# Performance work log

Measured on AMD Instinct MI355X. Metric: run time of the kernel, lower is better.

## Reference

```python
import jax, jax.numpy as jnp
import numpy as np

NUM_PERTS = 20000
D = 256          # embedding_dim
B, C = 64, 512   # batch_size, num_cells
EPS = 1e-5


def setup_inputs() -> dict:
    key = jax.random.key(0)
    ks = jax.random.split(key, 20)
    inp = {
        'perturbation_ids': jax.random.randint(ks[0], (B, C), 0, NUM_PERTS),
        'table': jax.random.normal(ks[1], (NUM_PERTS, D), dtype=jnp.float32),
    }
    s = 1.0 / np.sqrt(D)
    for i in range(4):
        inp[f'W{i+1}'] = jax.random.uniform(ks[2 + 2 * i], (D, D), minval=-s, maxval=s, dtype=jnp.float32)
        inp[f'b{i+1}'] = jax.random.uniform(ks[3 + 2 * i], (D,), minval=-s, maxval=s, dtype=jnp.float32)
    for i in range(3):
        inp[f'g{i+1}'] = jnp.ones((D,), jnp.float32)
        inp[f'be{i+1}'] = jnp.zeros((D,), jnp.float32)
    return inp


def _bn(x, gamma, beta):
    # BatchNorm1d forward with batch statistics (training-mode math, biased var)
    mu = jnp.mean(x, axis=0)
    var = jnp.mean(jnp.square(x - mu), axis=0)
    return (x - mu) * jax.lax.rsqrt(var + EPS) * gamma + beta


def reference(perturbation_ids, table,
              W1, b1, W2, b2, W3, b3, W4, b4,
              g1, be1, g2, be2, g3, be3):
    # Vectorized replacement of the Python double-loop dict gather
    emb = table[perturbation_ids]                 # (B, C, D)
    x = emb.reshape(-1, D)                        # (B*C, D)
    x = _bn(jax.nn.gelu(x @ W1 + b1, approximate=False), g1, be1)
    x = _bn(jax.nn.gelu(x @ W2 + b2, approximate=False), g2, be2)
    x = _bn(jax.nn.gelu(x @ W3 + b3, approximate=False), g3, be3)
    x = jax.nn.gelu(x @ W4 + b4, approximate=False)
    return x.reshape(B, C, D)
```

## Files before the change

### kernel.cpp

```cpp
#include <hip/hip_runtime.h>
#include <math.h>


typedef __attribute__((ext_vector_type(8))) short short8;
typedef __attribute__((ext_vector_type(4))) float floatx4;

#define DDIM 256
#define NBLK 512

struct Params {
    const int* ids;
    const float* table;
    const float* b[4];
    const float* g[3];
    const float* be[3];
    const unsigned short* Wt;
    float* stats;
    unsigned int* barrier;
    float* out;
};

__device__ __forceinline__ unsigned short f2bf(float f) {
    union { float f; unsigned int u; } v; v.f = f;
    unsigned int r = v.u + 0x7fffu + ((v.u >> 16) & 1u);
    return (unsigned short)(r >> 16);
}
__device__ __forceinline__ float bf2f(unsigned short u) {
    union { unsigned int i; float f; } v; v.i = ((unsigned int)u) << 16;
    return v.f;
}
__device__ __forceinline__ float gelu_fast(float x) {
    float z = 0.7978845608f * (x + 0.044715f * x * x * x);
    float e = __expf(2.0f * z);
    float th = 1.0f - 2.0f * __builtin_amdgcn_rcpf(1.0f + e);
    return 0.5f * x * (1.0f + th);
}

__global__ __launch_bounds__(256) void prep_kernel(
    const float* __restrict__ W0, const float* __restrict__ W1,
    const float* __restrict__ W2, const float* __restrict__ W3,
    unsigned short* __restrict__ Wt, float* __restrict__ stats,
    unsigned int* __restrict__ barrier)
{
    __shared__ unsigned short T[64][68];
    const int t = threadIdx.x, b = blockIdx.x;
    const int j  = b >> 4;
    const int kr = ((b >> 2) & 3) * 64;
    const int nc = (b & 3) * 64;
    const float* W = (j == 0) ? W0 : (j == 1) ? W1 : (j == 2) ? W2 : W3;

    {
        const int k = t >> 2, c0 = (t & 3) * 16;
        const float* src = W + (size_t)(kr + k) * DDIM + nc + c0;
#pragma unroll
        for (int i = 0; i < 4; ++i) {
            float4 v = *(const float4*)(src + i * 4);
            T[k][c0 + i * 4 + 0] = f2bf(v.x);
            T[k][c0 + i * 4 + 1] = f2bf(v.y);
            T[k][c0 + i * 4 + 2] = f2bf(v.z);
            T[k][c0 + i * 4 + 3] = f2bf(v.w);
        }
    }
    __syncthreads();
    {
        const int n = t >> 2, kc = (t & 3) * 16;
        union { unsigned short u[16]; uint4 v[2]; } o;
#pragma unroll
        for (int i = 0; i < 16; ++i) o.u[i] = T[kc + i][n];
        uint4* dst = (uint4*)(Wt + ((size_t)j << 16)
                              + (size_t)(nc + n) * DDIM + kr + kc);
        dst[0] = o.v[0]; dst[1] = o.v[1];
    }
    if (b < 48)       stats[b * 256 + t] = 0.f;
    else if (b < 52)  barrier[(b - 48) * 256 + t] = 0u;
}

__device__ __forceinline__ void grid_barrier(unsigned int* base, int phase)
{
    unsigned int* ph = base + phase * 256;
    __syncthreads();
    if (threadIdx.x == 0) {
        asm volatile("s_waitcnt vmcnt(0)" ::: "memory");
        unsigned int* gc   = ph + (blockIdx.x >> 6) * 16;
        unsigned int* root = ph + 128;
        unsigned int* flag = ph + 192;
        bool done = false;
        unsigned int old = __hip_atomic_fetch_add(gc, 1u, __ATOMIC_RELAXED,
                                                  __HIP_MEMORY_SCOPE_AGENT);
        if (old == 63u) {
            unsigned int r = __hip_atomic_fetch_add(root, 1u, __ATOMIC_RELAXED,
                                                    __HIP_MEMORY_SCOPE_AGENT);
            if (r == 7u) {
                __hip_atomic_store(flag, 1u, __ATOMIC_RELAXED,
                                   __HIP_MEMORY_SCOPE_AGENT);
                done = true;
            }
        }
        if (!done) {
            int cap = 2000000;
            while (!__hip_atomic_load(flag, __ATOMIC_RELAXED,
                                      __HIP_MEMORY_SCOPE_AGENT)) {
                __builtin_amdgcn_s_sleep(8);
                if (--cap == 0) break;
            }
        }
    }
    __syncthreads();
}

template<int GATHER, int AFFINE, int LAST>
__device__ __forceinline__ void layer_step(
    unsigned short* P, float* sc, float* sh,
    const Params& p,
    const unsigned short* Wt, const float* bias,
    const float* statsIn, const float* gma, const float* bta,
    float* statShards)
{
    const int tid  = threadIdx.x;
    const int blk  = blockIdx.x;
    const int wave = tid >> 6;
    const int lane = tid & 63;
    const int quad = lane >> 4;
    const int l15  = lane & 15;
    const int row0 = blk * 64;

    if (AFFINE) {
        if (tid < 256) {
            float sum = 0.f, sq = 0.f;
#pragma unroll
            for (int s = 0; s < 8; ++s) {
                sum += __hip_atomic_load(&statsIn[s * 512 + tid],
                                         __ATOMIC_RELAXED, __HIP_MEMORY_SCOPE_AGENT);
                sq  += __hip_atomic_load(&statsIn[s * 512 + 256 + tid],
                                         __ATOMIC_RELAXED, __HIP_MEMORY_SCOPE_AGENT);
            }
            const float mu  = sum * (1.f / 32768.f);
            const float var = sq * (1.f / 32768.f) - mu * mu;
            const float scl = rsqrtf(var + 1e-5f) * gma[tid];
            sc[tid] = scl;
            sh[tid] = bta[tid] - mu * scl;
        }
        __syncthreads();
    }

    {
        const int r     = tid >> 3;
        const int gbase = (tid & 7) * 4;
        if (GATHER) {
            const int src = p.ids[row0 + r];
            const float* tp = p.table + (size_t)src * DDIM + gbase * 8;
#pragma unroll
            for (int j = 0; j < 4; ++j) {
                float4 v0 = *(const float4*)(tp + j * 8);
                float4 v1 = *(const float4*)(tp + j * 8 + 4);
                union { unsigned short u[8]; uint4 v; } o;
                o.u[0]=f2bf(v0.x); o.u[1]=f2bf(v0.y); o.u[2]=f2bf(v0.z); o.u[3]=f2bf(v0.w);
                o.u[4]=f2bf(v1.x); o.u[5]=f2bf(v1.y); o.u[6]=f2bf(v1.z); o.u[7]=f2bf(v1.w);
                const int g = gbase + j;
                *(uint4*)(P + r * 256 + ((g ^ (r & 7)) << 3)) = o.v;
            }
        } else {
#pragma unroll
            for (int j = 0; j < 4; ++j) {
                const int g = gbase + j;
                unsigned short* slot = P + r * 256 + ((g ^ (r & 7)) << 3);
                union { unsigned short u[8]; uint4 v; } o;
                o.v = *(const uint4*)slot;
#pragma unroll
                for (int e = 0; e < 8; ++e) {
                    const int c = g * 8 + e;
                    o.u[e] = f2bf(fmaf(bf2f(o.u[e]), sc[c], sh[c]));
                }
                *(uint4*)slot = o.v;
            }
        }
    }

    float bias_v[2];
#pragma unroll
    for (int nt = 0; nt < 2; ++nt)
        bias_v[nt] = bias[wave * 32 + nt * 16 + l15];

    floatx4 acc[4][2];
#pragma unroll
    for (int i = 0; i < 4; ++i)
#pragma unroll
        for (int j = 0; j < 2; ++j)
            acc[i][j] = floatx4{0.f, 0.f, 0.f, 0.f};

    __syncthreads();

    const unsigned short* wb = Wt + (size_t)(wave * 32 + l15) * DDIM + quad * 8;
    short8 bfr[2], bnx[2], af[4], anx[4];
    {
        const int agp = (quad ^ (l15 & 7)) * 8;
#pragma unroll
        for (int nt = 0; nt < 2; ++nt)
            bfr[nt] = *(const short8*)(wb + (size_t)(nt * 16) * DDIM);
#pragma unroll
        for (int mt = 0; mt < 4; ++mt)
            af[mt] = *(const short8*)(P + (mt * 16 + l15) * 256 + agp);
    }
#pragma unroll
    for (int kk = 0; kk < 8; ++kk) {
        if (kk < 7) {
            const int agp = (((kk + 1) * 4 + quad) ^ (l15 & 7)) * 8;
#pragma unroll
            for (int nt = 0; nt < 2; ++nt)
                bnx[nt] = *(const short8*)(wb + (size_t)(nt * 16) * DDIM
                                           + (kk + 1) * 32);
#pragma unroll
            for (int mt = 0; mt < 4; ++mt)
                anx[mt] = *(const short8*)(P + (mt * 16 + l15) * 256 + agp);
        }
#pragma unroll
        for (int mt = 0; mt < 4; ++mt)
#pragma unroll
            for (int nt = 0; nt < 2; ++nt)
                acc[mt][nt] = __builtin_amdgcn_mfma_f32_16x16x32_bf16(
                    af[mt], bfr[nt], acc[mt][nt], 0, 0, 0);
#pragma unroll
        for (int x = 0; x < 4; ++x) af[x] = anx[x];
#pragma unroll
        for (int x = 0; x < 2; ++x) bfr[x] = bnx[x];
    }

    if (!LAST) __syncthreads();

    float s1[2] = {0.f, 0.f};
    float s2[2] = {0.f, 0.f};
#pragma unroll
    for (int mt = 0; mt < 4; ++mt) {
#pragma unroll
        for (int nt = 0; nt < 2; ++nt) {
            const int col = wave * 32 + nt * 16 + l15;
#pragma unroll
            for (int i = 0; i < 4; ++i) {
                const int r = mt * 16 + quad * 4 + i;
                float y = gelu_fast(acc[mt][nt][i] + bias_v[nt]);
                if (LAST) {
                    p.out[(size_t)(row0 + r) * DDIM + col] = y;
                } else {
                    const int g = col >> 3;
                    P[r * 256 + ((g ^ (r & 7)) << 3) + (col & 7)] = f2bf(y);
                    s1[nt] += y; s2[nt] += y * y;
                }
            }
        }
    }
    if (!LAST) {
#pragma unroll
        for (int nt = 0; nt < 2; ++nt) {
            s1[nt] += __shfl_xor(s1[nt], 16); s1[nt] += __shfl_xor(s1[nt], 32);
            s2[nt] += __shfl_xor(s2[nt], 16); s2[nt] += __shfl_xor(s2[nt], 32);
        }
        float* sb = statShards + (blk & 7) * 512;
        if (quad == 0) {
#pragma unroll
            for (int nt = 0; nt < 2; ++nt) {
                const int col = wave * 32 + nt * 16 + l15;
                atomicAdd(&sb[col],       s1[nt]);
                atomicAdd(&sb[256 + col], s2[nt]);
            }
        }
    }
}

__global__ __launch_bounds__(512, 4) void fused_enc(Params p)
{
    __shared__ alignas(16) unsigned short P[64 * 256];
    __shared__ float sc[256], sh[256];

    layer_step<1, 0, 0>(P, sc, sh, p, p.Wt,          p.b[0],
                        nullptr,         nullptr, nullptr, p.stats);
    grid_barrier(p.barrier, 0);
    layer_step<0, 1, 0>(P, sc, sh, p, p.Wt + 65536,  p.b[1],
                        p.stats,         p.g[0],  p.be[0], p.stats + 4096);
    grid_barrier(p.barrier, 1);
    layer_step<0, 1, 0>(P, sc, sh, p, p.Wt + 131072, p.b[2],
                        p.stats + 4096,  p.g[1],  p.be[1], p.stats + 8192);
    grid_barrier(p.barrier, 2);
    layer_step<0, 1, 1>(P, sc, sh, p, p.Wt + 196608, p.b[3],
                        p.stats + 8192,  p.g[2],  p.be[2], nullptr);
}

extern "C" void kernel_launch(void* const* d_in, const int* in_sizes, int n_in,
                              void* d_out, int out_size, void* d_ws, size_t ws_size,
                              hipStream_t stream)
{
    const float* W1 = (const float*)d_in[2];
    const float* W2 = (const float*)d_in[4];
    const float* W3 = (const float*)d_in[6];
    const float* W4 = (const float*)d_in[8];

    Params pp;
    pp.ids   = (const int*)  d_in[0];
    pp.table = (const float*)d_in[1];
    pp.b[0] = (const float*)d_in[3];
    pp.b[1] = (const float*)d_in[5];
    pp.b[2] = (const float*)d_in[7];
    pp.b[3] = (const float*)d_in[9];
    pp.g[0] = (const float*)d_in[10]; pp.be[0] = (const float*)d_in[11];
    pp.g[1] = (const float*)d_in[12]; pp.be[1] = (const float*)d_in[13];
    pp.g[2] = (const float*)d_in[14]; pp.be[2] = (const float*)d_in[15];

    unsigned char* ws = (unsigned char*)d_ws;
    unsigned short* Wt = (unsigned short*)ws;
    float* stats       = (float*)(ws + (size_t)524288);
    unsigned int* bar  = (unsigned int*)(ws + (size_t)589824);

    pp.Wt      = Wt;
    pp.stats   = stats;
    pp.barrier = bar;
    pp.out     = (float*)d_out;

    prep_kernel<<<64, 256, 0, stream>>>(W1, W2, W3, W4, Wt, stats, bar);
    fused_enc<<<dim3(NBLK), dim3(512), 0, stream>>>(pp);
}
```

Before: 167.4 us.

## Prefetch full next-layer weight slice into registers before grid barrier

Each wave now loads its whole 32-column weight slice for the next layer (16 short8 registers) right after the current layer's MFMA loop. That load then overlaps with the epilogue, stat atomics and grid barrier instead of being streamed inside the K loop. The first layer's weights are loaded at kernel start, overlapping the gather. It adds 64 VGPRs per thread, which under launch_bounds(512,4) could cause spills or lower occupancy.

```diff
diff --git a/kernel.cpp b/kernel.cpp
--- a/kernel.cpp
+++ b/kernel.cpp
@@ -108,11 +108,24 @@
     __syncthreads();
 }
 
+__device__ __forceinline__ void prefetch_B(short8 (&breg)[16],
+                                           const unsigned short* WtL,
+                                           int wave, int l15, int quad)
+{
+    const unsigned short* wb = WtL + (size_t)(wave * 32 + l15) * DDIM + quad * 8;
+#pragma unroll
+    for (int kk = 0; kk < 8; ++kk)
+#pragma unroll
+        for (int nt = 0; nt < 2; ++nt)
+            breg[kk * 2 + nt] =
+                *(const short8*)(wb + (size_t)(nt * 16) * DDIM + kk * 32);
+}
+
 template<int GATHER, int AFFINE, int LAST>
 __device__ __forceinline__ void layer_step(
     unsigned short* P, float* sc, float* sh,
-    const Params& p,
-    const unsigned short* Wt, const float* bias,
+    const Params& p, short8 (&breg)[16],
+    const unsigned short* WtNext, const float* bias,
     const float* statsIn, const float* gma, const float* bta,
     float* statShards)
 {
@@ -190,13 +203,9 @@
 
     __syncthreads();
 
-    const unsigned short* wb = Wt + (size_t)(wave * 32 + l15) * DDIM + quad * 8;
-    short8 bfr[2], bnx[2], af[4], anx[4];
+    short8 af[4], anx[4];
     {
         const int agp = (quad ^ (l15 & 7)) * 8;
-#pragma unroll
-        for (int nt = 0; nt < 2; ++nt)
-            bfr[nt] = *(const short8*)(wb + (size_t)(nt * 16) * DDIM);
 #pragma unroll
         for (int mt = 0; mt < 4; ++mt)
             af[mt] = *(const short8*)(P + (mt * 16 + l15) * 256 + agp);
@@ -206,10 +215,6 @@
         if (kk < 7) {
             const int agp = (((kk + 1) * 4 + quad) ^ (l15 & 7)) * 8;
 #pragma unroll
-            for (int nt = 0; nt < 2; ++nt)
-                bnx[nt] = *(const short8*)(wb + (size_t)(nt * 16) * DDIM
-                                           + (kk + 1) * 32);
-#pragma unroll
             for (int mt = 0; mt < 4; ++mt)
                 anx[mt] = *(const short8*)(P + (mt * 16 + l15) * 256 + agp);
         }
@@ -218,14 +223,14 @@
 #pragma unroll
             for (int nt = 0; nt < 2; ++nt)
                 acc[mt][nt] = __builtin_amdgcn_mfma_f32_16x16x32_bf16(
-                    af[mt], bfr[nt], acc[mt][nt], 0, 0, 0);
+                    af[mt], breg[kk * 2 + nt], acc[mt][nt], 0, 0, 0);
 #pragma unroll
         for (int x = 0; x < 4; ++x) af[x] = anx[x];
-#pragma unroll
-        for (int x = 0; x < 2; ++x) bfr[x] = bnx[x];
     }
 
     if (!LAST) __syncthreads();
+
+    if (!LAST) prefetch_B(breg, WtNext, wave, l15, quad);
 
     float s1[2] = {0.f, 0.f};
     float s2[2] = {0.f, 0.f};
@@ -271,16 +276,25 @@
     __shared__ alignas(16) unsigned short P[64 * 256];
     __shared__ float sc[256], sh[256];
 
-    layer_step<1, 0, 0>(P, sc, sh, p, p.Wt,          p.b[0],
+    const int tid  = threadIdx.x;
+    const int wave = tid >> 6;
+    const int lane = tid & 63;
+    const int quad = lane >> 4;
+    const int l15  = lane & 15;
+
+    short8 breg[16];
+    prefetch_B(breg, p.Wt, wave, l15, quad);
+
+    layer_step<1, 0, 0>(P, sc, sh, p, breg, p.Wt + 65536,  p.b[0],
                         nullptr,         nullptr, nullptr, p.stats);
     grid_barrier(p.barrier, 0);
-    layer_step<0, 1, 0>(P, sc, sh, p, p.Wt + 65536,  p.b[1],
+    layer_step<0, 1, 0>(P, sc, sh, p, breg, p.Wt + 131072, p.b[1],
                         p.stats,         p.g[0],  p.be[0], p.stats + 4096);
     grid_barrier(p.barrier, 1);
-    layer_step<0, 1, 0>(P, sc, sh, p, p.Wt + 131072, p.b[2],
+    layer_step<0, 1, 0>(P, sc, sh, p, breg, p.Wt + 196608, p.b[2],
                         p.stats + 4096,  p.g[1],  p.be[1], p.stats + 8192);
     grid_barrier(p.barrier, 2);
-    layer_step<0, 1, 1>(P, sc, sh, p, p.Wt + 196608, p.b[3],
+    layer_step<0, 1, 1>(P, sc, sh, p, breg, nullptr,       p.b[3],
                         p.stats + 8192,  p.g[2],  p.be[2], nullptr);
 }
 
```

Result: slower. 172.5 us (+3.0%).

## Keep GELU activations in registers across grid barrier and apply BN on writeback

Applied to the files above, without the earlier changes.

Post-GELU activations now stay in fp32 accumulator registers across the grid barrier instead of being written to LDS as bf16 before it. After the barrier the BatchNorm affine is applied straight from registers into the swizzled LDS tile. This removes one bf16 rounding, the LDS read-modify-write pass and a __syncthreads per layer. In exchange, the accumulators stay live across the grid barrier, which raises register pressure with launch_bounds(512,4).

```diff
diff --git a/kernel.cpp b/kernel.cpp
--- a/kernel.cpp
+++ b/kernel.cpp
@@ -108,10 +108,10 @@
     __syncthreads();
 }
 
-template<int GATHER, int AFFINE, int LAST>
+template<int GATHER, int LAST>
 __device__ __forceinline__ void layer_step(
     unsigned short* P, float* sc, float* sh,
-    const Params& p,
+    const Params& p, floatx4 (&acc)[4][2],
     const unsigned short* Wt, const float* bias,
     const float* statsIn, const float* gma, const float* bta,
     float* statShards)
@@ -124,7 +124,22 @@
     const int l15  = lane & 15;
     const int row0 = blk * 64;
 
-    if (AFFINE) {
+    if (GATHER) {
+        const int r     = tid >> 3;
+        const int gbase = (tid & 7) * 4;
+        const int src = p.ids[row0 + r];
+        const float* tp = p.table + (size_t)src * DDIM + gbase * 8;
+#pragma unroll
+        for (int j = 0; j < 4; ++j) {
+            float4 v0 = *(const float4*)(tp + j * 8);
+            float4 v1 = *(const float4*)(tp + j * 8 + 4);
+            union { unsigned short u[8]; uint4 v; } o;
+            o.u[0]=f2bf(v0.x); o.u[1]=f2bf(v0.y); o.u[2]=f2bf(v0.z); o.u[3]=f2bf(v0.w);
+            o.u[4]=f2bf(v1.x); o.u[5]=f2bf(v1.y); o.u[6]=f2bf(v1.z); o.u[7]=f2bf(v1.w);
+            const int g = gbase + j;
+            *(uint4*)(P + r * 256 + ((g ^ (r & 7)) << 3)) = o.v;
+        }
+    } else {
         if (tid < 256) {
             float sum = 0.f, sq = 0.f;
 #pragma unroll
@@ -141,37 +156,20 @@
             sh[tid] = bta[tid] - mu * scl;
         }
         __syncthreads();
-    }
-
-    {
-        const int r     = tid >> 3;
-        const int gbase = (tid & 7) * 4;
-        if (GATHER) {
-            const int src = p.ids[row0 + r];
-            const float* tp = p.table + (size_t)src * DDIM + gbase * 8;
-#pragma unroll
-            for (int j = 0; j < 4; ++j) {
-                float4 v0 = *(const float4*)(tp + j * 8);
-                float4 v1 = *(const float4*)(tp + j * 8 + 4);
-                union { unsigned short u[8]; uint4 v; } o;
-                o.u[0]=f2bf(v0.x); o.u[1]=f2bf(v0.y); o.u[2]=f2bf(v0.z); o.u[3]=f2bf(v0.w);
-                o.u[4]=f2bf(v1.x); o.u[5]=f2bf(v1.y); o.u[6]=f2bf(v1.z); o.u[7]=f2bf(v1.w);
-                const int g = gbase + j;
-                *(uint4*)(P + r * 256 + ((g ^ (r & 7)) << 3)) = o.v;
-            }
-        } else {
-#pragma unroll
-            for (int j = 0; j < 4; ++j) {
-                const int g = gbase + j;
-                unsigned short* slot = P + r * 256 + ((g ^ (r & 7)) << 3);
-                union { unsigned short u[8]; uint4 v; } o;
-                o.v = *(const uint4*)slot;
-#pragma unroll
-                for (int e = 0; e < 8; ++e) {
-                    const int c = g * 8 + e;
-                    o.u[e] = f2bf(fmaf(bf2f(o.u[e]), sc[c], sh[c]));
+
+#pragma unroll
+        for (int mt = 0; mt < 4; ++mt) {
+#pragma unroll
+            for (int nt = 0; nt < 2; ++nt) {
+                const int col = wave * 32 + nt * 16 + l15;
+                const float scl = sc[col], shf = sh[col];
+                const int gq = col >> 3, c7 = col & 7;
+#pragma unroll
+                for (int i = 0; i < 4; ++i) {
+                    const int r = mt * 16 + quad * 4 + i;
+                    const float a = fmaf(acc[mt][nt][i], scl, shf);
+                    P[r * 256 + ((gq ^ (r & 7)) << 3) + c7] = f2bf(a);
                 }
-                *(uint4*)slot = o.v;
             }
         }
     }
@@ -181,14 +179,13 @@
     for (int nt = 0; nt < 2; ++nt)
         bias_v[nt] = bias[wave * 32 + nt * 16 + l15];
 
-    floatx4 acc[4][2];
+    __syncthreads();
+
 #pragma unroll
     for (int i = 0; i < 4; ++i)
 #pragma unroll
         for (int j = 0; j < 2; ++j)
             acc[i][j] = floatx4{0.f, 0.f, 0.f, 0.f};
-
-    __syncthreads();
 
     const unsigned short* wb = Wt + (size_t)(wave * 32 + l15) * DDIM + quad * 8;
     short8 bfr[2], bnx[2], af[4], anx[4];
@@ -225,30 +222,32 @@
         for (int x = 0; x < 2; ++x) bfr[x] = bnx[x];
     }
 
-    if (!LAST) __syncthreads();
-
-    float s1[2] = {0.f, 0.f};
-    float s2[2] = {0.f, 0.f};
-#pragma unroll
-    for (int mt = 0; mt < 4; ++mt) {
-#pragma unroll
-        for (int nt = 0; nt < 2; ++nt) {
-            const int col = wave * 32 + nt * 16 + l15;
-#pragma unroll
-            for (int i = 0; i < 4; ++i) {
-                const int r = mt * 16 + quad * 4 + i;
-                float y = gelu_fast(acc[mt][nt][i] + bias_v[nt]);
-                if (LAST) {
-                    p.out[(size_t)(row0 + r) * DDIM + col] = y;
-                } else {
-                    const int g = col >> 3;
-                    P[r * 256 + ((g ^ (r & 7)) << 3) + (col & 7)] = f2bf(y);
+    if (LAST) {
+#pragma unroll
+        for (int mt = 0; mt < 4; ++mt)
+#pragma unroll
+            for (int nt = 0; nt < 2; ++nt) {
+                const int col = wave * 32 + nt * 16 + l15;
+#pragma unroll
+                for (int i = 0; i < 4; ++i) {
+                    const int r = mt * 16 + quad * 4 + i;
+                    p.out[(size_t)(row0 + r) * DDIM + col] =
+                        gelu_fast(acc[mt][nt][i] + bias_v[nt]);
+                }
+            }
+    } else {
+        float s1[2] = {0.f, 0.f};
+        float s2[2] = {0.f, 0.f};
+#pragma unroll
+        for (int mt = 0; mt < 4; ++mt)
+#pragma unroll
+            for (int nt = 0; nt < 2; ++nt)
+#pragma unroll
+                for (int i = 0; i < 4; ++i) {
+                    const float y = gelu_fast(acc[mt][nt][i] + bias_v[nt]);
+                    acc[mt][nt][i] = y;
                     s1[nt] += y; s2[nt] += y * y;
                 }
-            }
-        }
-    }
-    if (!LAST) {
 #pragma unroll
         for (int nt = 0; nt < 2; ++nt) {
             s1[nt] += __shfl_xor(s1[nt], 16); s1[nt] += __shfl_xor(s1[nt], 32);
@@ -271,17 +270,19 @@
     __shared__ alignas(16) unsigned short P[64 * 256];
     __shared__ float sc[256], sh[256];
 
-    layer_step<1, 0, 0>(P, sc, sh, p, p.Wt,          p.b[0],
-                        nullptr,         nullptr, nullptr, p.stats);
+    floatx4 acc[4][2];
+
+    layer_step<1, 0>(P, sc, sh, p, acc, p.Wt,          p.b[0],
+                     nullptr,         nullptr, nullptr, p.stats);
     grid_barrier(p.barrier, 0);
-    layer_step<0, 1, 0>(P, sc, sh, p, p.Wt + 65536,  p.b[1],
-                        p.stats,         p.g[0],  p.be[0], p.stats + 4096);
+    layer_step<0, 0>(P, sc, sh, p, acc, p.Wt + 65536,  p.b[1],
+                     p.stats,         p.g[0],  p.be[0], p.stats + 4096);
     grid_barrier(p.barrier, 1);
-    layer_step<0, 1, 0>(P, sc, sh, p, p.Wt + 131072, p.b[2],
-                        p.stats + 4096,  p.g[1],  p.be[1], p.stats + 8192);
+    layer_step<0, 0>(P, sc, sh, p, acc, p.Wt + 131072, p.b[2],
+                     p.stats + 4096,  p.g[1],  p.be[1], p.stats + 8192);
     grid_barrier(p.barrier, 2);
-    layer_step<0, 1, 1>(P, sc, sh, p, p.Wt + 196608, p.b[3],
-                        p.stats + 8192,  p.g[2],  p.be[2], nullptr);
+    layer_step<0, 1>(P, sc, sh, p, acc, p.Wt + 196608, p.b[3],
+                     p.stats + 8192,  p.g[2],  p.be[2], nullptr);
 }
 
 extern "C" void kernel_launch(void* const* d_in, const int* in_sizes, int n_in,
```

New measurement: 160.1 us (median of 3 runs). 1.05x faster.
